# Kernel optimization log

Hardware: AMD Instinct MI355X
Metric: run time of the kernel (lower is better)

Reference implementation:

```python
import jax, jax.numpy as jnp
import numpy as np

D_MODEL, H, DK, DV = 1024, 16, 64, 64
B, NQ, NK = 4, 1024, 1024
LN_EPS = 1e-5


def setup_inputs() -> dict:
    key = jax.random.key(0)
    ks = jax.random.split(key, 16)
    xavier = lambda k, i, o: jax.random.uniform(k, (i, o), jnp.float32,
                                                -np.sqrt(6.0 / (i + o)), np.sqrt(6.0 / (i + o)))
    return {
        "queries": jax.random.normal(ks[0], (B, NQ, D_MODEL), jnp.float32),
        "keys": jax.random.normal(ks[1], (B, NK, D_MODEL), jnp.float32),
        "values": jax.random.normal(ks[2], (B, NK, D_MODEL), jnp.float32),
        "geometry": jax.random.uniform(ks[3], (B, H, NQ, NK), jnp.float32),
        "attention_mask": jax.random.bernoulli(ks[4], 0.1, (B, H, NQ, NK)),
        "Wq": xavier(ks[5], D_MODEL, H * DK), "bq": jnp.zeros((H * DK,), jnp.float32),
        "Wk": xavier(ks[6], D_MODEL, H * DK), "bk": jnp.zeros((H * DK,), jnp.float32),
        "Wv": xavier(ks[7], D_MODEL, H * DV), "bv": jnp.zeros((H * DV,), jnp.float32),
        "Wo": xavier(ks[8], H * DV, D_MODEL), "bo": jnp.zeros((D_MODEL,), jnp.float32),
        "ln_gamma": jnp.ones((D_MODEL,), jnp.float32),
        "ln_beta": jnp.zeros((D_MODEL,), jnp.float32),
    }


def reference(queries, keys, values, geometry, attention_mask,
              Wq, bq, Wk, bk, Wv, bv, Wo, bo, ln_gamma, ln_beta):
    b, nq, _ = queries.shape
    nk = keys.shape[1]
    # QKV projections -> (b, h, n, d)
    q = (queries @ Wq + bq).reshape(b, nq, H, DK).transpose(0, 2, 1, 3)
    k = (keys @ Wk + bk).reshape(b, nk, H, DK).transpose(0, 2, 1, 3)
    v = (values @ Wv + bv).reshape(b, nk, H, DV).transpose(0, 2, 1, 3)
    att = jnp.einsum('bhqd,bhkd->bhqk', q, k) / np.sqrt(DK).astype(np.float32)
    att = jnp.where(attention_mask, -jnp.inf, att)
    # inline geometry log-bias before softmax
    w = jnp.log(jnp.clip(geometry, 1e-6)) + att
    w = jax.nn.softmax(w, axis=-1)  # dropout is identity in eval
    out = jnp.einsum('bhqk,bhkd->bqhd', w, v).reshape(b, nq, H * DV)
    out = out @ Wo + bo
    # residual + LayerNorm
    x = queries + out  # dropout identity in eval
    mu = jnp.mean(x, axis=-1, keepdims=True)
    var = jnp.mean((x - mu) ** 2, axis=-1, keepdims=True)
    return (x - mu) * jax.lax.rsqrt(var + LN_EPS) * ln_gamma + ln_beta
```

## Files before the change

kernel.cpp:

```cpp
#include <hip/hip_runtime.h>
#include <hip/hip_bf16.h>

typedef unsigned short u16;
typedef unsigned long long u64;
typedef __bf16 bf16x8 __attribute__((ext_vector_type(8)));
typedef float f32x4 __attribute__((ext_vector_type(4)));
typedef float f32x2 __attribute__((ext_vector_type(2)));

#define AS1 __attribute__((address_space(1)))
#define AS3 __attribute__((address_space(3)))
#define GLL16(gp, lp) __builtin_amdgcn_global_load_lds((AS1 const unsigned int*)(gp), (AS3 unsigned int*)(lp), 16, 0, 0)

__device__ __forceinline__ u16 f2bf(float f) {
    unsigned u = __builtin_bit_cast(unsigned, f);
    unsigned r = u + 0x7FFFu + ((u >> 16) & 1u);
    return (u16)(r >> 16);
}

__global__ void detect_kernel(const unsigned char* __restrict__ m, int* __restrict__ flag) {
    __shared__ int cnt1;
    __shared__ int big;
    if (threadIdx.x == 0) { cnt1 = 0; big = 0; }
    __syncthreads();
    int c1 = 0, bg = 0;
    for (int i = threadIdx.x; i < 16384; i += 256) {
        unsigned char v = m[i];
        if (v) {
            if ((i & 3) == 1) c1++;
            if (v > 1) bg++;
        }
    }
    atomicAdd(&cnt1, c1);
    atomicAdd(&big, bg);
    __syncthreads();
    if (threadIdx.x == 0) {
        int f;
        if (big == 0) f = cnt1 ? 0 : 1;
        else          f = cnt1 ? 3 : 2;
        *flag = f;
    }
}

#define MN_LOOP(PRED)                                                     \
    for (int row = wave; row < 65536; row += nw) {                        \
        size_t base = (size_t)row * 1024;                                 \
        u64 myw = 0;                                                      \
        _Pragma("unroll")                                                 \
        for (int kb = 0; kb < 16; ++kb) {                                 \
            size_t gi = base + kb * 64 + lane;                            \
            bool p = (PRED);                                              \
            u64 w = __ballot(p);                                          \
            if (lane == kb) myw = w;                                      \
        }                                                                 \
        if (lane < 16) MB[(size_t)row * 16 + lane] = myw;                 \
    }

__global__ __launch_bounds__(256) void masknorm_kernel(const void* __restrict__ mp,
                                                       const int* __restrict__ flagp,
                                                       u64* __restrict__ MB) {
    const int flag = *flagp;
    const int lane = threadIdx.x & 63;
    const int wave = blockIdx.x * 4 + (threadIdx.x >> 6);
    const int nw = gridDim.x * 4;
    if (flag == 0) {
        const unsigned char* m8 = (const unsigned char*)mp;
        MN_LOOP(m8[gi] != 0)
    } else if (flag == 1) {
        const int* m32 = (const int*)mp;
        MN_LOOP(m32[gi] != 0)
    } else if (flag == 2) {
        const unsigned* mf = (const unsigned*)mp;
        MN_LOOP((mf[gi] << 1) != 0)
    } else {
        const u16* mb = (const u16*)mp;
        MN_LOOP((mb[gi] & 0x7FFF) != 0)
    }
}

__global__ void cast3_kernel(const float* __restrict__ q, const float* __restrict__ k,
                             const float* __restrict__ v, u16* __restrict__ xq,
                             u16* __restrict__ xk, u16* __restrict__ xv) {
    const int n4 = 4 * 1024 * 1024 / 4;
    int stride = gridDim.x * blockDim.x;
    for (int i = blockIdx.x * blockDim.x + threadIdx.x; i < n4; i += stride) {
        float4 a = ((const float4*)q)[i];
        float4 b = ((const float4*)k)[i];
        float4 c = ((const float4*)v)[i];
        ((ushort4*)xq)[i] = make_ushort4(f2bf(a.x), f2bf(a.y), f2bf(a.z), f2bf(a.w));
        ((ushort4*)xk)[i] = make_ushort4(f2bf(b.x), f2bf(b.y), f2bf(b.z), f2bf(b.w));
        ((ushort4*)xv)[i] = make_ushort4(f2bf(c.x), f2bf(c.y), f2bf(c.z), f2bf(c.w));
    }
}

__global__ __launch_bounds__(256) void wtrans_kernel(
    const float* __restrict__ W0, const float* __restrict__ W1,
    const float* __restrict__ W2, const float* __restrict__ W3,
    u16* __restrict__ T0, u16* __restrict__ T1, u16* __restrict__ T2, u16* __restrict__ T3) {
    const float* W = (blockIdx.z == 0) ? W0 : (blockIdx.z == 1) ? W1 : (blockIdx.z == 2) ? W2 : W3;
    u16* T = (blockIdx.z == 0) ? T0 : (blockIdx.z == 1) ? T1 : (blockIdx.z == 2) ? T2 : T3;
    __shared__ float t[64][65];
    const int n0 = blockIdx.x * 64, k0 = blockIdx.y * 64;
    const int tx = threadIdx.x, ty = threadIdx.y;
    for (int j = ty; j < 64; j += 4) t[j][tx] = W[(size_t)(k0 + j) * 1024 + n0 + tx];
    __syncthreads();
    for (int j = ty; j < 64; j += 4) T[(size_t)(n0 + j) * 1024 + k0 + tx] = f2bf(t[tx][j]);
}

__global__ __launch_bounds__(256) void qkv_gemm(
    const u16* __restrict__ XQ, const u16* __restrict__ XK, const u16* __restrict__ XV,
    const u16* __restrict__ WQT, const u16* __restrict__ WKT, const u16* __restrict__ WVT,
    const float* __restrict__ bq, const float* __restrict__ bk, const float* __restrict__ bv,
    u16* __restrict__ QS, u16* __restrict__ KS, u16* __restrict__ VT) {
    __shared__ __align__(16) u16 lsA[128 * 64];
    __shared__ __align__(16) u16 lsB[128 * 64];
    const int z = blockIdx.z;
    const u16* A  = (z == 0) ? XQ : (z == 1) ? XK : XV;
    const u16* Bt = (z == 0) ? WQT : (z == 1) ? WKT : WVT;
    const float* bias = (z == 0) ? bq : (z == 1) ? bk : bv;
    const int tid = threadIdx.x, lane = tid & 63, wid = tid >> 6;
    const int bm = blockIdx.y, bn = blockIdx.x;
    const int wr = wid >> 1, wc = wid & 1;
    const int l15 = lane & 15, l4 = lane >> 4;
    f32x4 acc[4][4] = {};
    const int cbase = wid * 256;
    for (int t = 0; t < 16; ++t) {
        __syncthreads();
        for (int j = 0; j < 4; ++j) {
            int c = cbase + j * 64 + lane;
            int row = c >> 3, off = (c & 7) * 8;
            GLL16(A + (size_t)(bm * 128 + row) * 1024 + t * 64 + off, lsA + (size_t)(cbase + j * 64) * 8);
            GLL16(Bt + (size_t)(bn * 128 + row) * 1024 + t * 64 + off, lsB + (size_t)(cbase + j * 64) * 8);
        }
        __syncthreads();
        for (int kk = 0; kk < 2; ++kk) {
            bf16x8 af[4], bfr[4];
            for (int m = 0; m < 4; ++m)
                af[m] = *(const bf16x8*)(lsA + (wr * 64 + m * 16 + l15) * 64 + kk * 32 + l4 * 8);
            for (int n = 0; n < 4; ++n)
                bfr[n] = *(const bf16x8*)(lsB + (wc * 64 + n * 16 + l15) * 64 + kk * 32 + l4 * 8);
            for (int m = 0; m < 4; ++m)
                for (int n = 0; n < 4; ++n)
                    acc[m][n] = __builtin_amdgcn_mfma_f32_16x16x32_bf16(af[m], bfr[n], acc[m][n], 0, 0, 0);
        }
    }
    const float scale = (z == 0) ? 0.125f : 1.0f;
    for (int n = 0; n < 4; ++n) {
        int c = bn * 128 + wc * 64 + n * 16 + l15;
        float bv_ = bias[c];
        for (int m = 0; m < 4; ++m) {
            for (int j = 0; j < 4; ++j) {
                int r = bm * 128 + wr * 64 + m * 16 + l4 * 4 + j;
                float v = acc[m][n][j];
                if (z == 2) {
                    int bb = r >> 10, k = r & 1023, h = c >> 6, d = c & 63;
                    VT[((size_t)((bb * 16 + h) * 64 + d)) * 1024 + k] = f2bf(v + bv_);
                } else {
                    u16* outp = (z == 0) ? QS : KS;
                    outp[(size_t)r * 1024 + c] = f2bf((v + bv_) * scale);
                }
            }
        }
    }
}

__global__ __launch_bounds__(256) void gemm_out(
    const u16* __restrict__ A, const u16* __restrict__ Bt, const float* __restrict__ bias,
    float* __restrict__ outp, const float* __restrict__ resid) {
    __shared__ __align__(16) u16 lsA[128 * 64];
    __shared__ __align__(16) u16 lsB[128 * 64];
    const int tid = threadIdx.x, lane = tid & 63, wid = tid >> 6;
    const int bm = blockIdx.y, bn = blockIdx.x;
    const int wr = wid >> 1, wc = wid & 1;
    const int l15 = lane & 15, l4 = lane >> 4;
    f32x4 acc[4][4] = {};
    const int cbase = wid * 256;
    for (int t = 0; t < 16; ++t) {
        __syncthreads();
        for (int j = 0; j < 4; ++j) {
            int c = cbase + j * 64 + lane;
            int row = c >> 3, off = (c & 7) * 8;
            GLL16(A + (size_t)(bm * 128 + row) * 1024 + t * 64 + off, lsA + (size_t)(cbase + j * 64) * 8);
            GLL16(Bt + (size_t)(bn * 128 + row) * 1024 + t * 64 + off, lsB + (size_t)(cbase + j * 64) * 8);
        }
        __syncthreads();
        for (int kk = 0; kk < 2; ++kk) {
            bf16x8 af[4], bfr[4];
            for (int m = 0; m < 4; ++m)
                af[m] = *(const bf16x8*)(lsA + (wr * 64 + m * 16 + l15) * 64 + kk * 32 + l4 * 8);
            for (int n = 0; n < 4; ++n)
                bfr[n] = *(const bf16x8*)(lsB + (wc * 64 + n * 16 + l15) * 64 + kk * 32 + l4 * 8);
            for (int m = 0; m < 4; ++m)
                for (int n = 0; n < 4; ++n)
                    acc[m][n] = __builtin_amdgcn_mfma_f32_16x16x32_bf16(af[m], bfr[n], acc[m][n], 0, 0, 0);
        }
    }
    for (int n = 0; n < 4; ++n) {
        int c = bn * 128 + wc * 64 + n * 16 + l15;
        float bv = bias[c];
        for (int m = 0; m < 4; ++m)
            for (int j = 0; j < 4; ++j) {
                int r = bm * 128 + wr * 64 + m * 16 + l4 * 4 + j;
                outp[(size_t)r * 1024 + c] = acc[m][n][j] + bv + resid[(size_t)r * 1024 + c];
            }
    }
}

__global__ __launch_bounds__(256, 4) void attn_kernel(
    const u16* __restrict__ Qs, const u16* __restrict__ Ks, const u16* __restrict__ Vt,
    const float* __restrict__ geom, const u64* __restrict__ MBw,
    u16* __restrict__ AO) {
    __shared__ __align__(16) u16 lds[10240];

    const int g = blockIdx.x;
    const int tt = (g & 7) * 128 + (g >> 3);
    const int qb = tt & 15;
    const int bhid = tt >> 4;
    const int b = bhid >> 4, h = bhid & 15;
    const int q0 = qb * 64;

    const int tid = threadIdx.x, lane = tid & 63, wid = tid >> 6;
    const int l15 = lane & 15, l4 = lane >> 4;
    const int qrow = q0 + wid * 16;
    const size_t bh = (size_t)bhid;

    const u16* qp = Qs + (size_t)(b * 1024 + qrow + l15) * 1024 + h * 64 + l4 * 8;
    bf16x8 aq0 = *(const bf16x8*)qp;
    bf16x8 aq1 = *(const bf16x8*)(qp + 32);

    const int kr = tid >> 3, ks = tid & 7;
    const int kgr = (kr & 15) * 2 + (kr >> 4);
    const u16* ksrc = Ks + (size_t)(b * 1024 + kgr) * 1024 + h * 64 + ((ks ^ ((kr >> 1) & 7)) * 8);
    const int vr = tid >> 2, vs = tid & 3;
    const u16* vsrc = Vt + (bh * 64 + vr) * 1024 + ((vs ^ ((vr >> 1) & 3)) * 8);
    u16* const KD0 = lds + wid * 512;
    u16* const KD1 = lds + 2048 + wid * 512;
    u16* const VD0 = lds + 4096 + wid * 512;
    u16* const VD1 = lds + 6144 + wid * 512;
    u16* const pw  = lds + 8192 + wid * 512;

    const float* gbase = geom + (bh * 1024 + qrow + l4 * 4) * 1024 + l15 * 2;
    const unsigned* mb32 = (const unsigned*)(MBw + (bh * 1024 + qrow + l4 * 4) * 16);

    f32x4 o[4] = {};
    float m_run[4], l_run[4];
#pragma unroll
    for (int j = 0; j < 4; ++j) { m_run[j] = -1e30f; l_run[j] = 0.f; }

    f32x2 gpA[4], gpB[4];
    unsigned mkA[4], mkB[4];

    GLL16(ksrc, KD0);
    GLL16(vsrc, VD0);
    __builtin_amdgcn_sched_barrier(0);
#pragma unroll
    for (int j = 0; j < 4; ++j) {
        gpA[j] = *(const f32x2*)(gbase + j * 1024);
        mkA[j] = mb32[j * 32];
    }
    __builtin_amdgcn_sched_barrier(0);
    asm volatile("s_waitcnt vmcnt(8)" ::: "memory");
    __builtin_amdgcn_sched_barrier(0);
    __builtin_amdgcn_s_barrier();
    __builtin_amdgcn_sched_barrier(0);

#define BODY(T, GC, GN, MC, MN, KBC, VBC, KDN, VDN)                                      \
    do {                                                                                 \
        if ((T) + 1 < 32) {                                                              \
            GLL16(ksrc + (size_t)((T) + 1) * 32768, KDN);                                \
            GLL16(vsrc + ((T) + 1) * 32, VDN);                                           \
            __builtin_amdgcn_sched_barrier(0);                                           \
            _Pragma("unroll")                                                            \
            for (int j = 0; j < 4; ++j) {                                                \
                GN[j] = *(const f32x2*)(gbase + j * 1024 + ((T) + 1) * 32);              \
                MN[j] = mb32[j * 32 + (T) + 1];                                          \
            }                                                                            \
            __builtin_amdgcn_sched_barrier(0);                                           \
        }                                                                                \
        f32x4 s0, s1;                                                                    \
        {                                                                                \
            const int rr = l15, swz = (rr >> 1) & 7;                                     \
            bf16x8 k0 = *(const bf16x8*)((KBC) + rr * 64 + ((l4 ^ swz) * 8));            \
            bf16x8 k1 = *(const bf16x8*)((KBC) + rr * 64 + (((4 + l4) ^ swz) * 8));      \
            f32x4 z = {};                                                                \
            z = __builtin_amdgcn_mfma_f32_16x16x32_bf16(aq0, k0, z, 0, 0, 0);            \
            s0 = __builtin_amdgcn_mfma_f32_16x16x32_bf16(aq1, k1, z, 0, 0, 0);           \
        }                                                                                \
        {                                                                                \
            const int rr = 16 + l15, swz = (rr >> 1) & 7;                                \
            bf16x8 k0 = *(const bf16x8*)((KBC) + rr * 64 + ((l4 ^ swz) * 8));            \
            bf16x8 k1 = *(const bf16x8*)((KBC) + rr * 64 + (((4 + l4) ^ swz) * 8));      \
            f32x4 z = {};                                                                \
            z = __builtin_amdgcn_mfma_f32_16x16x32_bf16(aq0, k0, z, 0, 0, 0);            \
            s1 = __builtin_amdgcn_mfma_f32_16x16x32_bf16(aq1, k1, z, 0, 0, 0);           \
        }                                                                                \
        float sclv[4];                                                                   \
        _Pragma("unroll")                                                                \
        for (int j = 0; j < 4; ++j) {                                                    \
            float a0 = s0[j], a1 = s1[j];                                                \
            float mt = fmaxf(a0, a1);                                                    \
            mt = fmaxf(mt, __shfl_xor(mt, 1, 16));                                       \
            mt = fmaxf(mt, __shfl_xor(mt, 2, 16));                                       \
            mt = fmaxf(mt, __shfl_xor(mt, 4, 16));                                       \
            mt = fmaxf(mt, __shfl_xor(mt, 8, 16));                                       \
            float mn = fmaxf(m_run[j], mt);                                              \
            float scl = __expf(m_run[j] - mn);                                           \
            m_run[j] = mn;                                                               \
            unsigned mb2 = (MC[j] >> (l15 * 2)) & 3u;                                    \
            f32x2 gv = GC[j];                                                            \
            float p0 = (mb2 & 1u) ? 0.f : __expf(a0 - mn) * fmaxf(gv[0], 1e-6f);         \
            float p1 = (mb2 & 2u) ? 0.f : __expf(a1 - mn) * fmaxf(gv[1], 1e-6f);         \
            float rs = p0 + p1;                                                          \
            rs += __shfl_xor(rs, 1, 16);                                                 \
            rs += __shfl_xor(rs, 2, 16);                                                 \
            rs += __shfl_xor(rs, 4, 16);                                                 \
            rs += __shfl_xor(rs, 8, 16);                                                 \
            l_run[j] = l_run[j] * scl + rs;                                              \
            sclv[j] = scl;                                                               \
            const int row = l4 * 4 + j;                                                  \
            const int slot4 = (l15 & 3) | ((((l15 >> 2) ^ l4) & 3) << 2);                \
            unsigned pk = (unsigned)f2bf(p0) | ((unsigned)f2bf(p1) << 16);               \
            *(unsigned*)(pw + row * 32 + slot4 * 2) = pk;                                \
        }                                                                                \
        _Pragma("unroll")                                                                \
        for (int df = 0; df < 4; ++df) {                                                 \
            f32x4 tv = o[df];                                                            \
            _Pragma("unroll")                                                            \
            for (int j = 0; j < 4; ++j) tv[j] *= sclv[j];                                \
            o[df] = tv;                                                                  \
        }                                                                                \
        {                                                                                \
            const int blk = (l4 ^ (l15 >> 2)) & 3;                                       \
            bf16x8 pa = *(const bf16x8*)(pw + l15 * 32 + blk * 8);                       \
            _Pragma("unroll")                                                            \
            for (int df = 0; df < 4; ++df) {                                             \
                const int rr = df * 16 + l15, vswz = (rr >> 1) & 3;                      \
                bf16x8 v0 = *(const bf16x8*)((VBC) + rr * 32 + ((l4 ^ vswz) * 8));       \
                o[df] = __builtin_amdgcn_mfma_f32_16x16x32_bf16(pa, v0, o[df], 0, 0, 0); \
            }                                                                            \
        }                                                                                \
        if ((T) + 1 < 32) {                                                              \
            asm volatile("s_waitcnt vmcnt(8)" ::: "memory");                             \
            __builtin_amdgcn_sched_barrier(0);                                           \
            __builtin_amdgcn_s_barrier();                                                \
            __builtin_amdgcn_sched_barrier(0);                                           \
        }                                                                                \
    } while (0)

    for (int it = 0; it < 16; ++it) {
        const int t0 = it * 2;
        BODY(t0,     gpA, gpB, mkA, mkB, (lds + 0),    (lds + 4096), KD1, VD1);
        BODY(t0 + 1, gpB, gpA, mkB, mkA, (lds + 2048), (lds + 6144), KD0, VD0);
    }
#undef BODY

    float inv[4];
#pragma unroll
    for (int j = 0; j < 4; ++j) inv[j] = 1.0f / l_run[j];
#pragma unroll
    for (int p = 0; p < 2; ++p) {
#pragma unroll
        for (int df2 = 0; df2 < 2; ++df2) {
            const int df = p * 2 + df2;
#pragma unroll
            for (int j = 0; j < 4; ++j)
                pw[(l4 * 4 + j) * 32 + df2 * 16 + l15] = f2bf(o[df][j] * inv[j]);
        }
        const int er = lane >> 2, ec = lane & 3;
        bf16x8 val = *(const bf16x8*)(pw + er * 32 + ec * 8);
        *(bf16x8*)(AO + (size_t)(b * 1024 + qrow + er) * 1024 + h * 64 + p * 32 + ec * 8) = val;
    }
}

__global__ __launch_bounds__(256) void ln_kernel(const float* __restrict__ Y,
                                                 const float* __restrict__ gamma,
                                                 const float* __restrict__ beta,
                                                 float* __restrict__ out) {
    __shared__ float red[8];
    const int r = blockIdx.x, tid = threadIdx.x, lane = tid & 63, wid = tid >> 6;
    float4 v = ((const float4*)(Y + (size_t)r * 1024))[tid];
    float s = v.x + v.y + v.z + v.w;
    float q = v.x * v.x + v.y * v.y + v.z * v.z + v.w * v.w;
    for (int d = 1; d < 64; d <<= 1) {
        s += __shfl_xor(s, d, 64);
        q += __shfl_xor(q, d, 64);
    }
    if (lane == 0) { red[wid] = s; red[4 + wid] = q; }
    __syncthreads();
    float ts = red[0] + red[1] + red[2] + red[3];
    float tq = red[4] + red[5] + red[6] + red[7];
    float mu = ts * (1.f / 1024.f);
    float var = tq * (1.f / 1024.f) - mu * mu;
    float rstd = rsqrtf(var + 1e-5f);
    float4 gg = ((const float4*)gamma)[tid];
    float4 be = ((const float4*)beta)[tid];
    float4 ov;
    ov.x = (v.x - mu) * rstd * gg.x + be.x;
    ov.y = (v.y - mu) * rstd * gg.y + be.y;
    ov.z = (v.z - mu) * rstd * gg.z + be.z;
    ov.w = (v.w - mu) * rstd * gg.w + be.w;
    ((float4*)(out + (size_t)r * 1024))[tid] = ov;
}

extern "C" void kernel_launch(void* const* d_in, const int* in_sizes, int n_in,
                              void* d_out, int out_size, void* d_ws, size_t ws_size,
                              hipStream_t stream) {
    const float* queries = (const float*)d_in[0];
    const float* keys    = (const float*)d_in[1];
    const float* values  = (const float*)d_in[2];
    const float* geom    = (const float*)d_in[3];
    const void*  mask    = d_in[4];
    const float* Wq = (const float*)d_in[5];  const float* bq = (const float*)d_in[6];
    const float* Wk = (const float*)d_in[7];  const float* bk = (const float*)d_in[8];
    const float* Wv = (const float*)d_in[9];  const float* bv = (const float*)d_in[10];
    const float* Wo = (const float*)d_in[11]; const float* bo = (const float*)d_in[12];
    const float* gamma = (const float*)d_in[13];
    const float* beta  = (const float*)d_in[14];

    char* ws = (char*)d_ws;
    const size_t MB_ = 1024 * 1024;
    u16* XQ  = (u16*)(ws + 0);
    u16* XK  = (u16*)(ws + 8 * MB_);
    u16* XV  = (u16*)(ws + 16 * MB_);
    u16* WQT = (u16*)(ws + 24 * MB_);
    u16* WKT = (u16*)(ws + 26 * MB_);
    u16* WVT = (u16*)(ws + 28 * MB_);
    u16* WOT = (u16*)(ws + 30 * MB_);
    u16* QS  = (u16*)(ws + 32 * MB_);
    u16* KS  = (u16*)(ws + 40 * MB_);
    u16* VT  = (u16*)(ws + 48 * MB_);
    u16* AO  = (u16*)(ws + 56 * MB_);
    u64* MBITS = (u64*)(ws + 16 * MB_);
    float* Y = (float*)(ws + 0);
    int* FLAG = (int*)(ws + 64 * MB_);

    detect_kernel<<<1, 256, 0, stream>>>((const unsigned char*)mask, FLAG);
    cast3_kernel<<<1024, 256, 0, stream>>>(queries, keys, values, XQ, XK, XV);
    wtrans_kernel<<<dim3(16, 16, 4), dim3(64, 4), 0, stream>>>(Wq, Wk, Wv, Wo, WQT, WKT, WVT, WOT);
    qkv_gemm<<<dim3(8, 32, 3), 256, 0, stream>>>(XQ, XK, XV, WQT, WKT, WVT, bq, bk, bv, QS, KS, VT);
    masknorm_kernel<<<4096, 256, 0, stream>>>(mask, FLAG, MBITS);
    attn_kernel<<<1024, 256, 0, stream>>>(QS, KS, VT, geom, MBITS, AO);
    gemm_out<<<dim3(8, 32), 256, 0, stream>>>(AO, WOT, bo, Y, queries);
    ln_kernel<<<4096, 256, 0, stream>>>(Y, gamma, beta, (float*)d_out);
}
```

Before: 308.2 us.

## Triple-buffer K/V tiles in attention and raise MFMA wave priority

Moves the attention kernel's K/V LDS staging from double to triple buffering, so loads are issued two tiles ahead and the vmcnt waits are retuned to match. The loop is unrolled by six to rotate the three buffers, with a peeled tail for the last two tiles. MFMA sections are wrapped in s_setprio to favour matrix issue. This costs more LDS per block (28KB), which may limit occupancy, and the wait counts must match the outstanding loads exactly.

```diff
diff --git a/kernel.cpp b/kernel.cpp
--- a/kernel.cpp
+++ b/kernel.cpp
@@ -209,7 +209,7 @@
     const u16* __restrict__ Qs, const u16* __restrict__ Ks, const u16* __restrict__ Vt,
     const float* __restrict__ geom, const u64* __restrict__ MBw,
     u16* __restrict__ AO) {
-    __shared__ __align__(16) u16 lds[10240];
+    __shared__ __align__(16) u16 lds[14336];
 
     const int g = blockIdx.x;
     const int tt = (g & 7) * 128 + (g >> 3);
@@ -232,11 +232,13 @@
     const u16* ksrc = Ks + (size_t)(b * 1024 + kgr) * 1024 + h * 64 + ((ks ^ ((kr >> 1) & 7)) * 8);
     const int vr = tid >> 2, vs = tid & 3;
     const u16* vsrc = Vt + (bh * 64 + vr) * 1024 + ((vs ^ ((vr >> 1) & 3)) * 8);
-    u16* const KD0 = lds + wid * 512;
+    u16* const KD0 = lds + 0    + wid * 512;
     u16* const KD1 = lds + 2048 + wid * 512;
-    u16* const VD0 = lds + 4096 + wid * 512;
-    u16* const VD1 = lds + 6144 + wid * 512;
-    u16* const pw  = lds + 8192 + wid * 512;
+    u16* const KD2 = lds + 4096 + wid * 512;
+    u16* const VD0 = lds + 6144 + 0    + wid * 512;
+    u16* const VD1 = lds + 6144 + 2048 + wid * 512;
+    u16* const VD2 = lds + 6144 + 4096 + wid * 512;
+    u16* const pw  = lds + 12288 + wid * 512;
 
     const float* gbase = geom + (bh * 1024 + qrow + l4 * 4) * 1024 + l15 * 2;
     const unsigned* mb32 = (const unsigned*)(MBw + (bh * 1024 + qrow + l4 * 4) * 16);
@@ -251,6 +253,8 @@
 
     GLL16(ksrc, KD0);
     GLL16(vsrc, VD0);
+    GLL16(ksrc + 32768, KD1);
+    GLL16(vsrc + 32, VD1);
     __builtin_amdgcn_sched_barrier(0);
 #pragma unroll
     for (int j = 0; j < 4; ++j) {
@@ -258,17 +262,19 @@
         mkA[j] = mb32[j * 32];
     }
     __builtin_amdgcn_sched_barrier(0);
-    asm volatile("s_waitcnt vmcnt(8)" ::: "memory");
+    asm volatile("s_waitcnt vmcnt(10)" ::: "memory");
     __builtin_amdgcn_sched_barrier(0);
     __builtin_amdgcn_s_barrier();
     __builtin_amdgcn_sched_barrier(0);
 
-#define BODY(T, GC, GN, MC, MN, KBC, VBC, KDN, VDN)                                      \
+#define BODY(T, GC, GN, MC, MN, KBC, VBC, KDN, VDN, WSTR)                                \
     do {                                                                                 \
+        if ((T) + 2 < 32) {                                                              \
+            GLL16(ksrc + (size_t)((T) + 2) * 32768, KDN);                                \
+            GLL16(vsrc + ((T) + 2) * 32, VDN);                                           \
+            __builtin_amdgcn_sched_barrier(0);                                           \
+        }                                                                                \
         if ((T) + 1 < 32) {                                                              \
-            GLL16(ksrc + (size_t)((T) + 1) * 32768, KDN);                                \
-            GLL16(vsrc + ((T) + 1) * 32, VDN);                                           \
-            __builtin_amdgcn_sched_barrier(0);                                           \
             _Pragma("unroll")                                                            \
             for (int j = 0; j < 4; ++j) {                                                \
                 GN[j] = *(const f32x2*)(gbase + j * 1024 + ((T) + 1) * 32);              \
@@ -277,6 +283,7 @@
             __builtin_amdgcn_sched_barrier(0);                                           \
         }                                                                                \
         f32x4 s0, s1;                                                                    \
+        __builtin_amdgcn_s_setprio(1);                                                   \
         {                                                                                \
             const int rr = l15, swz = (rr >> 1) & 7;                                     \
             bf16x8 k0 = *(const bf16x8*)((KBC) + rr * 64 + ((l4 ^ swz) * 8));            \
@@ -293,6 +300,7 @@
             z = __builtin_amdgcn_mfma_f32_16x16x32_bf16(aq0, k0, z, 0, 0, 0);            \
             s1 = __builtin_amdgcn_mfma_f32_16x16x32_bf16(aq1, k1, z, 0, 0, 0);           \
         }                                                                                \
+        __builtin_amdgcn_s_setprio(0);                                                   \
         float sclv[4];                                                                   \
         _Pragma("unroll")                                                                \
         for (int j = 0; j < 4; ++j) {                                                    \
@@ -331,26 +339,34 @@
         {                                                                                \
             const int blk = (l4 ^ (l15 >> 2)) & 3;                                       \
             bf16x8 pa = *(const bf16x8*)(pw + l15 * 32 + blk * 8);                       \
+            __builtin_amdgcn_s_setprio(1);                                               \
             _Pragma("unroll")                                                            \
             for (int df = 0; df < 4; ++df) {                                             \
                 const int rr = df * 16 + l15, vswz = (rr >> 1) & 3;                      \
                 bf16x8 v0 = *(const bf16x8*)((VBC) + rr * 32 + ((l4 ^ vswz) * 8));       \
                 o[df] = __builtin_amdgcn_mfma_f32_16x16x32_bf16(pa, v0, o[df], 0, 0, 0); \
             }                                                                            \
+            __builtin_amdgcn_s_setprio(0);                                               \
         }                                                                                \
         if ((T) + 1 < 32) {                                                              \
-            asm volatile("s_waitcnt vmcnt(8)" ::: "memory");                             \
+            asm volatile(WSTR ::: "memory");                                             \
             __builtin_amdgcn_sched_barrier(0);                                           \
             __builtin_amdgcn_s_barrier();                                                \
             __builtin_amdgcn_sched_barrier(0);                                           \
         }                                                                                \
     } while (0)
 
-    for (int it = 0; it < 16; ++it) {
-        const int t0 = it * 2;
-        BODY(t0,     gpA, gpB, mkA, mkB, (lds + 0),    (lds + 4096), KD1, VD1);
-        BODY(t0 + 1, gpB, gpA, mkB, mkA, (lds + 2048), (lds + 6144), KD0, VD0);
-    }
+    for (int it = 0; it < 5; ++it) {
+        const int t0 = it * 6;
+        BODY(t0 + 0, gpA, gpB, mkA, mkB, (lds + 0),    (lds + 6144),        KD2, VD2, "s_waitcnt vmcnt(10)");
+        BODY(t0 + 1, gpB, gpA, mkB, mkA, (lds + 2048), (lds + 6144 + 2048), KD0, VD0, "s_waitcnt vmcnt(10)");
+        BODY(t0 + 2, gpA, gpB, mkA, mkB, (lds + 4096), (lds + 6144 + 4096), KD1, VD1, "s_waitcnt vmcnt(10)");
+        BODY(t0 + 3, gpB, gpA, mkB, mkA, (lds + 0),    (lds + 6144),        KD2, VD2, "s_waitcnt vmcnt(10)");
+        BODY(t0 + 4, gpA, gpB, mkA, mkB, (lds + 2048), (lds + 6144 + 2048), KD0, VD0, "s_waitcnt vmcnt(10)");
+        BODY(t0 + 5, gpB, gpA, mkB, mkA, (lds + 4096), (lds + 6144 + 4096), KD1, VD1, "s_waitcnt vmcnt(10)");
+    }
+    BODY(30, gpA, gpB, mkA, mkB, (lds + 0),    (lds + 6144),        KD2, VD2, "s_waitcnt vmcnt(8)");
+    BODY(31, gpB, gpA, mkB, mkA, (lds + 2048), (lds + 6144 + 2048), KD0, VD0, "s_waitcnt vmcnt(8)");
 #undef BODY
 
     float inv[4];
```

After: 309.1 us. No clear change (+0.3%).
